# Performance work log

Measured on AMD Instinct MI355X. Metric: run time of the kernel, lower is better.

The kernel has to match this reference:

```python
import jax, jax.numpy as jnp
import numpy as np

L, D, H, F = 6, 1024, 8, 2048
B, S, IN = 4, 2048, 128
DK = D // H
EPS = 1e-6


def layer_norm(x, s, b):
    mu = jnp.mean(x, -1, keepdims=True)
    var = jnp.mean((x - mu) ** 2, -1, keepdims=True)
    return (x - mu) * jax.lax.rsqrt(var + EPS) * s + b


def rotate_every_two(x):
    x1 = x[..., ::2]
    x2 = x[..., 1::2]
    return jnp.stack([-x2, x1], axis=-1).reshape(x.shape)


def rotary_tables():
    # torchscale RetNet xpos-style angles: each freq repeated twice (interleaved)
    angle = 1.0 / (10000.0 ** jnp.linspace(0.0, 1.0, DK // 2))
    angle = jnp.repeat(angle, 2)                      # [DK]
    idx = jnp.arange(S, dtype=jnp.float32)[:, None]   # [S,1]
    return jnp.sin(idx * angle), jnp.cos(idx * angle)  # [S,DK] each


def decay_mask():
    # gamma_h = 1 - 2^(-5-h); D[h,n,m] = gamma_h^(n-m) for n>=m else 0,
    # row-normalized by sqrt(row sum) as in torchscale.
    gamma = 1.0 - 2.0 ** (-5.0 - jnp.arange(H, dtype=jnp.float32))  # [H]
    n = jnp.arange(S)
    diff = jnp.clip(n[:, None] - n[None, :], 0)                      # [S,S]
    tril = n[:, None] >= n[None, :]
    m = jnp.where(tril[None], gamma[:, None, None] ** diff[None].astype(jnp.float32), 0.0)
    return m / jnp.sqrt(jnp.sum(m, -1, keepdims=True))               # [H,S,S]


def setup_inputs() -> dict:
    key = jax.random.key(0)
    ks = iter(jax.random.split(key, 24))
    p = lambda shape: jax.random.normal(next(ks), shape, jnp.float32) * 0.02
    return {
        "x": jax.random.normal(next(ks), (B, S, IN), jnp.float32),
        "W_in": p((IN, D)), "b_in": jnp.zeros((D,), jnp.float32),
        "Wq": p((L, D, D)), "Wk": p((L, D, D)), "Wv": p((L, D, D)),
        "Wg": p((L, D, D)), "Wo": p((L, D, D)),
        "gn_g": jnp.ones((L, D), jnp.float32),
        "ln1_s": jnp.ones((L, D), jnp.float32), "ln1_b": jnp.zeros((L, D), jnp.float32),
        "ffn_W1": p((L, D, F)), "ffn_b1": jnp.zeros((L, F), jnp.float32),
        "ffn_W2": p((L, F, D)), "ffn_b2": jnp.zeros((L, D), jnp.float32),
        "ln2_s": jnp.ones((L, D), jnp.float32), "ln2_b": jnp.zeros((L, D), jnp.float32),
        "lnf_s": jnp.ones((D,), jnp.float32), "lnf_b": jnp.zeros((D,), jnp.float32),
        "W_reg": p((D, 1)), "b_reg": jnp.zeros((1,), jnp.float32),
    }


def reference(x, W_in, b_in, Wq, Wk, Wv, Wg, Wo, gn_g, ln1_s, ln1_b,
              ffn_W1, ffn_b1, ffn_W2, ffn_b2, ln2_s, ln2_b, lnf_s, lnf_b,
              W_reg, b_reg):
    sin, cos = rotary_tables()
    dmask = decay_mask()  # [H,S,S]
    h = x @ W_in + b_in   # input_embed
    for l in range(L):
        # --- multi-scale retention (pre-norm) ---
        y = layer_norm(h, ln1_s[l], ln1_b[l])
        q = (y @ Wq[l]).reshape(B, S, H, DK).transpose(0, 2, 1, 3)
        k = (y @ Wk[l]).reshape(B, S, H, DK).transpose(0, 2, 1, 3) * (DK ** -0.5)
        v = (y @ Wv[l]).reshape(B, S, H, DK).transpose(0, 2, 1, 3)
        q = q * cos + rotate_every_two(q) * sin
        k = k * cos + rotate_every_two(k) * sin
        scores = jnp.einsum('bhnd,bhmd->bhnm', q, k)
        ret = scores * dmask[None]
        ret = ret / jnp.clip(jnp.abs(ret).sum(-1, keepdims=True), 1.0, None)
        o = jnp.einsum('bhnm,bhmd->bhnd', ret, v)
        # per-head group (RMS) norm
        o = o * jax.lax.rsqrt(jnp.mean(o * o, -1, keepdims=True) + EPS)
        o = o.transpose(0, 2, 1, 3).reshape(B, S, D) * gn_g[l]
        g = y @ Wg[l]
        h = h + (jax.nn.silu(g) * o) @ Wo[l]
        # --- FFN (pre-norm) ---
        y = layer_norm(h, ln2_s[l], ln2_b[l])
        h = h + jax.nn.gelu(y @ ffn_W1[l] + ffn_b1[l]) @ ffn_W2[l] + ffn_b2[l]
    h = layer_norm(h, lnf_s, lnf_b)
    out = 1.1 * jax.nn.sigmoid(h @ W_reg + b_reg) - 0.05
    return out.squeeze(-1)  # [B,S]
```

## Files before the change

### kernel.cpp

```cpp
#include <hip/hip_runtime.h>

#define L_ 6
#define D_ 1024
#define H_ 8
#define F_ 2048
#define B_ 4
#define S_ 2048
#define IN_ 128
#define DK_ 128
#define BS_ (B_*S_)
#define D2_ 4096

typedef short bf16x8 __attribute__((ext_vector_type(8)));
typedef float f32x4 __attribute__((ext_vector_type(4)));

__device__ inline float b2f(unsigned short u){ union{unsigned int i; float f;} v; v.i = ((unsigned int)u)<<16; return v.f; }
__device__ inline unsigned short f2b(float f){ union{unsigned int i; float f;} v; v.f = f; unsigned int r = v.i + 0x7FFFu + ((v.i>>16)&1u); return (unsigned short)(r>>16); }
__device__ inline unsigned int cvtpk(float lo, float hi){
    unsigned int r; asm("v_cvt_pk_bf16_f32 %0, %1, %2" : "=v"(r) : "v"(lo), "v"(hi)); return r;
}

__device__ inline void gld16(const void* g, void* l) {
    __builtin_amdgcn_global_load_lds((const __attribute__((address_space(1))) unsigned int*)g,
                                     (__attribute__((address_space(3))) unsigned int*)l, 16, 0, 0);
}

#define GBAR() do{ asm volatile("" ::: "memory"); __builtin_amdgcn_s_barrier(); asm volatile("" ::: "memory"); }while(0)

__global__ void f32_to_bf16_k(const float* __restrict__ in, unsigned short* __restrict__ out, int n)
{
    int i = blockIdx.x*256 + threadIdx.x;
    if (i < n) out[i] = f2b(in[i]);
}

__global__ void transpose_w_k(const float* __restrict__ in, unsigned short* __restrict__ out, int R, int C, size_t ostride)
{
    __shared__ float tile[32][33];
    int z = blockIdx.z;
    const float* pi = in + (size_t)z*R*C;
    unsigned short* po = out + (size_t)z*ostride;
    int c0 = blockIdx.x*32, r0 = blockIdx.y*32;
    int tx = threadIdx.x, ty = threadIdx.y;
    #pragma unroll
    for (int i=0;i<4;i++) tile[ty+i*8][tx] = pi[(size_t)(r0+ty+i*8)*C + c0+tx];
    __syncthreads();
    #pragma unroll
    for (int i=0;i<4;i++) po[(size_t)(c0+ty+i*8)*R + r0+tx] = f2b(tile[tx][ty+i*8]);
}

__global__ void transpose_v_k(const unsigned short* __restrict__ vb, unsigned short* __restrict__ vT)
{
    __shared__ unsigned short tile[32][33];
    int z = blockIdx.z;
    int b = z >> 3, hh = z & 7;
    int s0 = blockIdx.x*32, d0 = blockIdx.y*32;
    int tx = threadIdx.x, ty = threadIdx.y;
    #pragma unroll
    for (int i=0;i<4;i++) tile[ty+i*8][tx] = vb[(size_t)(b*S_ + s0+ty+i*8)*D2_ + hh*DK_ + d0+tx];
    __syncthreads();
    #pragma unroll
    for (int i=0;i<4;i++) vT[((size_t)z*DK_ + d0+ty+i*8)*S_ + s0+tx] = tile[tx][ty+i*8];
}

__global__ void build_sincos_k(float* __restrict__ cost, float* __restrict__ sint)
{
    int id = blockIdx.x*256 + threadIdx.x;
    int s = id >> 6, i = id & 63;
    float ang = powf(10000.f, -(float)i/63.f);
    float a = (float)s * ang;
    float sv = sinf(a), cv = cosf(a);
    sint[s*DK_ + 2*i] = sv; sint[s*DK_ + 2*i+1] = sv;
    cost[s*DK_ + 2*i] = cv; cost[s*DK_ + 2*i+1] = cv;
}

__global__ void build_dnorm_k(float* __restrict__ dnorm)
{
    int id = blockIdx.x*256 + threadIdx.x;
    int h = id >> 11, n = id & (S_-1);
    double g = 1.0 - exp2((double)(-5 - h));
    double sum = (1.0 - exp(((double)(n+1))*log(g))) / (1.0 - g);
    dnorm[id] = (float)(1.0/sqrt(sum));
}

__device__ inline float bsum(float v, float* red, int t)
{
    #pragma unroll
    for (int m=32; m; m>>=1) v += __shfl_xor(v, m);
    __syncthreads();
    if ((t & 63) == 0) red[t>>6] = v;
    __syncthreads();
    return red[0]+red[1]+red[2]+red[3];
}

__global__ __launch_bounds__(256) void ln_to_bf16_k(const float* __restrict__ x, const float* __restrict__ s,
                                                    const float* __restrict__ b, unsigned short* __restrict__ y)
{
    __shared__ float red[4];
    int row = blockIdx.x, t = threadIdx.x;
    const float* xr = x + (size_t)row * D_;
    float4 v = ((const float4*)xr)[t];
    float mu = bsum(v.x+v.y+v.z+v.w, red, t) * (1.f/D_);
    float d0=v.x-mu, d1=v.y-mu, d2=v.z-mu, d3=v.w-mu;
    float var = bsum(d0*d0+d1*d1+d2*d2+d3*d3, red, t) * (1.f/D_);
    float inv = rsqrtf(var + 1e-6f);
    int c = t*4;
    float o0 = d0*inv*s[c+0] + b[c+0];
    float o1 = d1*inv*s[c+1] + b[c+1];
    float o2 = d2*inv*s[c+2] + b[c+2];
    float o3 = d3*inv*s[c+3] + b[c+3];
    unsigned long long pk = (unsigned long long)f2b(o0) | ((unsigned long long)f2b(o1)<<16)
                          | ((unsigned long long)f2b(o2)<<32) | ((unsigned long long)f2b(o3)<<48);
    *(unsigned long long*)(y + (size_t)row*D_ + c) = pk;
}

template<int MODE, int BN>
__global__ __launch_bounds__(512, 2)
void gemm6(const unsigned short* __restrict__ A,
           const unsigned short* __restrict__ Bt,
           const float* __restrict__ bias,
           void* __restrict__ Cv,
           int M, int N, int K)
{
    constexpr int BM   = 256;
    constexpr int IR   = 8;
    constexpr int JR   = BN/64;
    constexpr int ASUB = BM*64;
    constexpr int BSUB = BN*64;
    constexpr int BUFSZ= 2*ASUB + 2*BSUB;
    constexpr int AP   = 2;
    constexpr int BP   = BN/128;
    __shared__ unsigned char lds[2*BUFSZ];

    const int tid = threadIdx.x, lane = tid & 63, w = tid >> 6;
    const int r16 = lane & 15, quad = (lane >> 4) & 3;
    const int wm = w >> 2, wn = w & 3;

    const int nwg = (int)(gridDim.x * gridDim.y);
    int bid = (int)(blockIdx.y * gridDim.x + blockIdx.x);
    if ((nwg & 7) == 0) bid = (bid & 7) * (nwg >> 3) + (bid >> 3);
    const int m0 = (bid / (int)gridDim.x) * BM;
    const int n0 = (bid % (int)gridDim.x) * BN;

    const int srow = tid >> 2;
    const int schk = (tid & 3) ^ ((tid >> 3) & 3);
    const unsigned short* gA = A  + (size_t)(m0 + srow) * K + schk*8;
    const unsigned short* gB = Bt + (size_t)(n0 + srow) * K + schk*8;

    const int rchk = (quad ^ ((r16 >> 1) & 3)) * 16;
    const int aoff = (wm*128 + r16)*64 + rchk;
    const int boff = (wn*(BN/4) + r16)*64 + rchk;

    f32x4 acc[IR][JR];
    #pragma unroll
    for (int i=0;i<IR;i++)
      #pragma unroll
      for (int j=0;j<JR;j++) acc[i][j] = (f32x4){0.f,0.f,0.f,0.f};

    const int NT = K >> 6;

    auto stageA = [&](int t, int kk){
        unsigned char* dst = lds + (t&1)*BUFSZ + kk*ASUB;
        const unsigned short* src = gA + (size_t)t*64 + kk*32;
        #pragma unroll
        for (int p=0;p<AP;p++)
            gld16(src + (size_t)(p*128)*K, dst + p*8192 + tid*16);
    };
    auto stageB = [&](int t, int kk){
        unsigned char* dst = lds + (t&1)*BUFSZ + 2*ASUB + kk*BSUB;
        const unsigned short* src = gB + (size_t)t*64 + kk*32;
        #pragma unroll
        for (int p=0;p<BP;p++)
            gld16(src + (size_t)(p*128)*K, dst + p*8192 + tid*16);
    };

    stageA(0,0); stageB(0,0); stageA(0,1); stageB(0,1);
    if constexpr (BN==256) asm volatile("s_waitcnt vmcnt(4)" ::: "memory");
    else                   asm volatile("s_waitcnt vmcnt(3)" ::: "memory");
    GBAR();

    for (int t = 0; t < NT; ++t) {
        const unsigned char* cb = lds + (t&1)*BUFSZ;
        const bool pre = (t+1 < NT);
        #pragma unroll
        for (int kk = 0; kk < 2; ++kk) {
            const unsigned char* ak = cb + kk*ASUB;
            const unsigned char* bk = cb + 2*ASUB + kk*BSUB;
            if constexpr (BN == 256) {
                bf16x8 af[4], bg[JR];
                #pragma unroll
                for (int i=0;i<4;i++) af[i] = *(const bf16x8*)(ak + aoff + i*1024);
                #pragma unroll
                for (int j=0;j<JR;j++) bg[j] = *(const bf16x8*)(bk + boff + j*1024);
                if (pre) stageA(t+1, kk);
                GBAR();
                asm volatile("s_waitcnt lgkmcnt(0)" ::: "memory");
                __builtin_amdgcn_s_setprio(1);
                #pragma unroll
                for (int i=0;i<4;i++)
                  #pragma unroll
                  for (int j=0;j<JR;j++)
                    acc[i][j] = __builtin_amdgcn_mfma_f32_16x16x32_bf16(af[i], bg[j], acc[i][j], 0,0,0);
                __builtin_amdgcn_s_setprio(0);
                GBAR();
                #pragma unroll
                for (int i=0;i<4;i++) af[i] = *(const bf16x8*)(ak + aoff + (4+i)*1024);
                if (pre) stageB(t+1, kk);
                GBAR();
                asm volatile("s_waitcnt lgkmcnt(0)" ::: "memory");
                __builtin_amdgcn_s_setprio(1);
                #pragma unroll
                for (int i=0;i<4;i++)
                  #pragma unroll
                  for (int j=0;j<JR;j++)
                    acc[4+i][j] = __builtin_amdgcn_mfma_f32_16x16x32_bf16(af[i], bg[j], acc[4+i][j], 0,0,0);
                __builtin_amdgcn_s_setprio(0);
                if (pre) asm volatile("s_waitcnt vmcnt(4)" ::: "memory");
                else     asm volatile("s_waitcnt vmcnt(0)" ::: "memory");
                GBAR();
            } else {
                bf16x8 af[8], bg[JR];
                #pragma unroll
                for (int i=0;i<8;i++) af[i] = *(const bf16x8*)(ak + aoff + i*1024);
                #pragma unroll
                for (int j=0;j<JR;j++) bg[j] = *(const bf16x8*)(bk + boff + j*1024);
                if (pre) { stageA(t+1, kk); stageB(t+1, kk); }
                GBAR();
                asm volatile("s_waitcnt lgkmcnt(0)" ::: "memory");
                __builtin_amdgcn_s_setprio(1);
                #pragma unroll
                for (int i=0;i<8;i++)
                  #pragma unroll
                  for (int j=0;j<JR;j++)
                    acc[i][j] = __builtin_amdgcn_mfma_f32_16x16x32_bf16(af[i], bg[j], acc[i][j], 0,0,0);
                __builtin_amdgcn_s_setprio(0);
                if (pre) asm volatile("s_waitcnt vmcnt(3)" ::: "memory");
                else     asm volatile("s_waitcnt vmcnt(0)" ::: "memory");
                GBAR();
            }
        }
    }

    float* Cf = (float*)Cv;
    unsigned short* Cb = (unsigned short*)Cv;
    float bvs[JR];
    #pragma unroll
    for (int j=0;j<JR;j++) bvs[j] = bias ? bias[n0 + wn*(BN/4) + j*16 + r16] : 0.f;
    #pragma unroll
    for (int i=0;i<IR;i++) {
      #pragma unroll
      for (int r=0;r<4;r++) {
        const size_t crow = (size_t)(m0 + wm*128 + i*16 + quad*4 + r);
        #pragma unroll
        for (int j=0;j<JR;j++) {
          const int ccol = n0 + wn*(BN/4) + j*16 + r16;
          float v = acc[i][j][r];
          if (MODE == 0) { Cf[crow*N + ccol] = v + bvs[j]; }
          else if (MODE == 1) { Cf[crow*N + ccol] += v + bvs[j]; }
          else if (MODE == 2) { Cb[crow*N + ccol] = f2b(v); }
          else {
            v += bvs[j];
            float t3 = tanhf(0.7978845608028654f*(v + 0.044715f*v*v*v));
            Cb[crow*N + ccol] = f2b(0.5f*v*(1.f + t3));
          }
        }
      }
    }
}

__global__ __launch_bounds__(256) void rope_qk_k(unsigned short* __restrict__ qkvg,
                                                 const float* __restrict__ cost, const float* __restrict__ sint)
{
    int id = blockIdx.x*256 + threadIdx.x;
    int row = id >> 9;
    int d = (id & 511) * 2;
    int s = row & (S_-1);
    int dk = d & (DK_-1);
    float c0 = cost[s*DK_ + dk],   s0 = sint[s*DK_ + dk];
    float c1 = cost[s*DK_ + dk+1], s1 = sint[s*DK_ + dk+1];
    size_t off = (size_t)row*D2_ + d;
    unsigned int qu = *(unsigned int*)(qkvg + off);
    float q0 = b2f((unsigned short)(qu & 0xffffu)), q1 = b2f((unsigned short)(qu >> 16));
    float r0 = q0*c0 - q1*s0;
    float r1 = q1*c1 + q0*s1;
    *(unsigned int*)(qkvg + off) = (unsigned int)f2b(r0) | ((unsigned int)f2b(r1) << 16);
    const float sc = 0.08838834764831845f;
    unsigned int ku = *(unsigned int*)(qkvg + off + 1024);
    float k0 = b2f((unsigned short)(ku & 0xffffu))*sc, k1 = b2f((unsigned short)(ku >> 16))*sc;
    float t0 = k0*c0 - k1*s0;
    float t1 = k1*c1 + k0*s1;
    *(unsigned int*)(qkvg + off + 1024) = (unsigned int)f2b(t0) | ((unsigned int)f2b(t1) << 16);
}

__global__ __launch_bounds__(256, 2) void retention_k(const unsigned short* __restrict__ qk_base,
    const unsigned short* __restrict__ vT, const float* __restrict__ dnorm,
    const float* __restrict__ gng, unsigned short* __restrict__ attnin)
{
    __shared__ __align__(16) unsigned char lds[75776];
    const int Lf = (int)(blockIdx.y * gridDim.x + blockIdx.x);
    const int kx = Lf & 7, mm = Lf >> 3;
    const int bh = 4*kx + (mm >> 4);
    const int pr = mm & 15;
    const int b = bh >> 3, hh = bh & 7;
    const int tid = threadIdx.x, lane = tid & 63, w = tid >> 6;
    const int r16 = lane & 15, quad = lane >> 4;

    const float l2g = log2f(1.f - exp2f(-5.f - (float)hh));
    const int ithr = (int)(45.f / (-l2g));
    const unsigned int mkr = (r16 & 7) << 4;

    const int mk2  = ((tid >> 4) & 7) << 4;
    const int mkv2 = ((tid >> 3) & 7) << 4;
    const unsigned short* ksrc = qk_base + 1024 + ((size_t)(b*S_) + (tid>>4))*D2_ + hh*DK_
                                + ((((tid&15)*16) ^ mk2) >> 1);
    const unsigned short* vsrc = vT + ((size_t)bh*DK_ + (tid>>3))*S_ + ((((tid&7)*16) ^ mkv2) >> 1);

    float Aarr[4];
    #pragma unroll
    for (int r=0;r<4;r++) Aarr[r] = exp2f(l2g * (float)(63 - (w*16 + quad*4 + r)));

    float* dsums = (float*)(lds + 73728);
    float* ssums = (float*)(lds + 74752);

    auto stage = [&](int c2, int kt2){
        const unsigned short* s0 = ksrc + (size_t)kt2*64*D2_;
        #pragma unroll
        for (int i=0;i<4;i++)
            gld16(s0 + (size_t)i*16*D2_, lds + c2*16384 + i*4096 + w*1024);
        const unsigned short* s1 = vsrc + kt2*64;
        #pragma unroll
        for (int j=0;j<4;j++)
            gld16(s1 + (size_t)j*32*S_, lds + 32768 + c2*16384 + j*4096 + w*1024);
    };

    int cur = 0;

    #pragma unroll 1
    for (int seg = 0; seg < 2; ++seg) {
        const int qt = seg ? pr : (31 - pr);
        const int n0 = qt * 64;
        const int kt_start = max(0, (n0 - ithr) >> 6);

        bf16x8 qf[4][4];
        const unsigned short* qptr = qk_base + ((size_t)(b*S_ + n0 + r16))*D2_ + hh*DK_;
        #pragma unroll
        for (int qtl=0;qtl<4;qtl++)
          #pragma unroll
          for (int c=0;c<4;c++) qf[qtl][c] = *(const bf16x8*)(qptr + qtl*16*D2_ + c*32 + quad*8);

        f32x4 oacc[4][2];
        #pragma unroll
        for (int qtl=0;qtl<4;qtl++)
          #pragma unroll
          for (int dt=0;dt<2;dt++) oacc[qtl][dt] = (f32x4){0.f,0.f,0.f,0.f};
        float dsum[4] = {0.f,0.f,0.f,0.f};

        stage(cur, kt_start);

        #pragma unroll 1
        for (int kt = kt_start; kt <= qt; ++kt) {
            if (kt < qt) { stage(cur^1, kt+1); asm volatile("s_waitcnt vmcnt(8)" ::: "memory"); }
            else         { asm volatile("s_waitcnt vmcnt(0)" ::: "memory"); }
            GBAR();

            const unsigned char* kb = lds + cur*16384;
            bf16x8 kf[4];
            #pragma unroll
            for (int c=0;c<4;c++)
                kf[c] = *(const bf16x8*)(kb + (w*16 + r16)*256 + ((c*64 + quad*16) ^ mkr));
            f32x4 sf[4];
            #pragma unroll
            for (int qtl=0;qtl<4;qtl++) sf[qtl] = (f32x4){0.f,0.f,0.f,0.f};
            __builtin_amdgcn_s_setprio(1);
            #pragma unroll
            for (int c=0;c<4;c++)
              #pragma unroll
              for (int qtl=0;qtl<4;qtl++)
                sf[qtl] = __builtin_amdgcn_mfma_f32_16x16x32_bf16(kf[c], qf[qtl][c], sf[qtl], 0,0,0);
            __builtin_amdgcn_s_setprio(0);

            const bool diag = (kt == qt);
            #pragma unroll
            for (int qtl=0;qtl<4;qtl++) {
                float Bq = exp2f(l2g * (float)(n0 + qtl*16 + r16 - kt*64 - 63));
                float pv[4];
                #pragma unroll
                for (int r=0;r<4;r++) {
                    float p = sf[qtl][r] * Aarr[r] * Bq;
                    if (diag && (w*16 + quad*4 + r > qtl*16 + r16)) p = 0.f;
                    dsum[qtl] += fabsf(p);
                    pv[r] = p;
                }
                unsigned long long pk = (unsigned long long)cvtpk(pv[0], pv[1])
                                      | ((unsigned long long)cvtpk(pv[2], pv[3]) << 32);
                *(unsigned long long*)(lds + 65536 + (qtl*16 + r16)*128 + ((w*32 + quad*8) ^ mkr)) = pk;
            }
            asm volatile("s_waitcnt lgkmcnt(0)" ::: "memory");
            GBAR();

            const unsigned char* vb = lds + 32768 + cur*16384;
            bf16x8 pa[4][2], vf[2][2];
            #pragma unroll
            for (int qtl=0;qtl<4;qtl++)
              #pragma unroll
              for (int ks=0;ks<2;ks++)
                pa[qtl][ks] = *(const bf16x8*)(lds + 65536 + (qtl*16 + r16)*128 + ((ks*64 + quad*16) ^ mkr));
            #pragma unroll
            for (int dt=0;dt<2;dt++)
              #pragma unroll
              for (int ks=0;ks<2;ks++)
                vf[dt][ks] = *(const bf16x8*)(vb + (w*32 + dt*16 + r16)*128 + ((ks*64 + quad*16) ^ mkr));
            __builtin_amdgcn_s_setprio(1);
            #pragma unroll
            for (int qtl=0;qtl<4;qtl++)
              #pragma unroll
              for (int dt=0;dt<2;dt++)
                #pragma unroll
                for (int ks=0;ks<2;ks++)
                  oacc[qtl][dt] = __builtin_amdgcn_mfma_f32_16x16x32_bf16(pa[qtl][ks], vf[dt][ks], oacc[qtl][dt], 0,0,0);
            __builtin_amdgcn_s_setprio(0);
            GBAR();
            cur ^= 1;
        }

        #pragma unroll
        for (int qtl=0;qtl<4;qtl++) {
            float dv = dsum[qtl];
            dv += __shfl_xor(dv, 16); dv += __shfl_xor(dv, 32);
            if (lane < 16) dsums[w*64 + qtl*16 + r16] = dv;
        }
        __syncthreads();
        float scl[4][4], pss[4][4];
        #pragma unroll
        for (int qtl=0;qtl<4;qtl++) {
            #pragma unroll
            for (int r=0;r<4;r++) {
                int nl = qtl*16 + quad*4 + r;
                float dv = dsums[nl] + dsums[64+nl] + dsums[128+nl] + dsums[192+nl];
                float nr = dnorm[hh*S_ + n0 + nl];
                float sc = nr / fmaxf(1.f, dv * nr);
                scl[qtl][r] = sc;
                float s2 = 0.f;
                #pragma unroll
                for (int dt=0;dt<2;dt++) { float t = oacc[qtl][dt][r]*sc; s2 += t*t; }
                s2 += __shfl_xor(s2,1); s2 += __shfl_xor(s2,2);
                s2 += __shfl_xor(s2,4); s2 += __shfl_xor(s2,8);
                pss[qtl][r] = s2;
            }
        }
        if (r16 == 0) {
            #pragma unroll
            for (int qtl=0;qtl<4;qtl++)
              #pragma unroll
              for (int r=0;r<4;r++)
                ssums[w*64 + qtl*16 + quad*4 + r] = pss[qtl][r];
        }
        __syncthreads();
        #pragma unroll
        for (int qtl=0;qtl<4;qtl++) {
            float rms[4];
            #pragma unroll
            for (int r=0;r<4;r++) {
                int nl = qtl*16 + quad*4 + r;
                float s2 = ssums[nl] + ssums[64+nl] + ssums[128+nl] + ssums[192+nl];
                rms[r] = rsqrtf(s2*(1.f/DK_) + 1e-6f);
            }
            #pragma unroll
            for (int dt=0;dt<2;dt++) {
                int d = w*32 + dt*16 + r16;
                float gg = gng[hh*DK_ + d];
                #pragma unroll
                for (int r=0;r<4;r++) {
                    int n = n0 + qtl*16 + quad*4 + r;
                    float gv = b2f(qk_base[(size_t)(b*S_ + n)*D2_ + 3072 + hh*DK_ + d]);
                    float sg = gv / (1.f + expf(-gv));
                    float ov = oacc[qtl][dt][r]*scl[qtl][r]*rms[r]*gg;
                    attnin[(size_t)(b*S_ + n)*D_ + hh*DK_ + d] = f2b(ov*sg);
                }
            }
        }
        __syncthreads();
    }
}

__global__ __launch_bounds__(256) void head_out_k(const float* __restrict__ h, const float* __restrict__ s,
    const float* __restrict__ b, const float* __restrict__ wreg, const float* __restrict__ breg,
    float* __restrict__ out)
{
    __shared__ float red[4];
    int row = blockIdx.x, t = threadIdx.x;
    const float* xr = h + (size_t)row*D_;
    float4 v = ((const float4*)xr)[t];
    float mu = bsum(v.x+v.y+v.z+v.w, red, t) * (1.f/D_);
    float d0=v.x-mu, d1=v.y-mu, d2=v.z-mu, d3=v.w-mu;
    float var = bsum(d0*d0+d1*d1+d2*d2+d3*d3, red, t) * (1.f/D_);
    float inv = rsqrtf(var + 1e-6f);
    int c = t*4;
    float dot = (d0*inv*s[c+0]+b[c+0])*wreg[c+0] + (d1*inv*s[c+1]+b[c+1])*wreg[c+1]
              + (d2*inv*s[c+2]+b[c+2])*wreg[c+2] + (d3*inv*s[c+3]+b[c+3])*wreg[c+3];
    dot = bsum(dot, red, t);
    if (t == 0) out[row] = 1.1f / (1.f + expf(-(dot + breg[0]))) - 0.05f;
}

extern "C" void kernel_launch(void* const* d_in, const int* in_sizes, int n_in,
                              void* d_out, int out_size, void* d_ws, size_t ws_size,
                              hipStream_t stream)
{
    (void)in_sizes; (void)n_in; (void)out_size; (void)ws_size;
    const float* x    = (const float*)d_in[0];
    const float* W_in = (const float*)d_in[1];
    const float* b_in = (const float*)d_in[2];
    const float* Wq   = (const float*)d_in[3];
    const float* Wk   = (const float*)d_in[4];
    const float* Wv   = (const float*)d_in[5];
    const float* Wg   = (const float*)d_in[6];
    const float* Wo   = (const float*)d_in[7];
    const float* gn_g = (const float*)d_in[8];
    const float* ln1s = (const float*)d_in[9];
    const float* ln1b = (const float*)d_in[10];
    const float* W1   = (const float*)d_in[11];
    const float* b1   = (const float*)d_in[12];
    const float* W2   = (const float*)d_in[13];
    const float* b2   = (const float*)d_in[14];
    const float* ln2s = (const float*)d_in[15];
    const float* ln2b = (const float*)d_in[16];
    const float* lnfs = (const float*)d_in[17];
    const float* lnfb = (const float*)d_in[18];
    const float* Wreg = (const float*)d_in[19];
    const float* breg = (const float*)d_in[20];

    char* ws = (char*)d_ws;
    size_t off = 0;
    auto alloc = [&](size_t bytes) { char* p = ws + off; off += (bytes + 255) & ~(size_t)255; return p; };

    const size_t DD = (size_t)D_*D_;
    unsigned short* wqkvgT = (unsigned short*)alloc((size_t)L_*4*DD*2);
    unsigned short* woT  = (unsigned short*)alloc((size_t)L_*DD*2);
    unsigned short* w1T  = (unsigned short*)alloc((size_t)L_*D_*F_*2);
    unsigned short* w2T  = (unsigned short*)alloc((size_t)L_*D_*F_*2);
    unsigned short* winT = (unsigned short*)alloc((size_t)D_*IN_*2);
    unsigned short* x_bf = (unsigned short*)alloc((size_t)BS_*IN_*2);
    float*          hbuf = (float*)alloc((size_t)BS_*D_*4);
    unsigned short* y_bf = (unsigned short*)alloc((size_t)BS_*D_*2);
    unsigned short* qkvg = (unsigned short*)alloc((size_t)BS_*D2_*2);
    unsigned short* vTb  = (unsigned short*)alloc((size_t)BS_*D_*2);
    float*          cost = (float*)alloc((size_t)S_*DK_*4);
    float*          sint = (float*)alloc((size_t)S_*DK_*4);
    float*          dnrm = (float*)alloc((size_t)H_*S_*4);
    unsigned short* attn = y_bf;
    unsigned short* midb = qkvg;

    dim3 tb(32, 8);

    f32_to_bf16_k<<<(BS_*IN_)/256, 256, 0, stream>>>(x, x_bf, BS_*IN_);
    transpose_w_k<<<dim3(32,32,L_), tb, 0, stream>>>(Wq, wqkvgT + 0*DD, D_, D_, 4*DD);
    transpose_w_k<<<dim3(32,32,L_), tb, 0, stream>>>(Wk, wqkvgT + 1*DD, D_, D_, 4*DD);
    transpose_w_k<<<dim3(32,32,L_), tb, 0, stream>>>(Wv, wqkvgT + 2*DD, D_, D_, 4*DD);
    transpose_w_k<<<dim3(32,32,L_), tb, 0, stream>>>(Wg, wqkvgT + 3*DD, D_, D_, 4*DD);
    transpose_w_k<<<dim3(32,32,L_), tb, 0, stream>>>(Wo, woT, D_, D_, DD);
    transpose_w_k<<<dim3(64,32,L_), tb, 0, stream>>>(W1, w1T, D_, F_, (size_t)D_*F_);
    transpose_w_k<<<dim3(32,64,L_), tb, 0, stream>>>(W2, w2T, F_, D_, (size_t)D_*F_);
    transpose_w_k<<<dim3(32, 4, 1), tb, 0, stream>>>(W_in, winT, IN_, D_, (size_t)D_*IN_);
    build_sincos_k<<<(S_*64)/256, 256, 0, stream>>>(cost, sint);
    build_dnorm_k<<<(H_*S_)/256, 256, 0, stream>>>(dnrm);

    gemm6<0,128><<<dim3(D_/128, BS_/256), 512, 0, stream>>>(x_bf, winT, b_in, hbuf, BS_, D_, IN_);

    for (int l = 0; l < L_; ++l) {
        ln_to_bf16_k<<<BS_, 256, 0, stream>>>(hbuf, ln1s + l*D_, ln1b + l*D_, y_bf);
        gemm6<2,256><<<dim3(D2_/256, BS_/256), 512, 0, stream>>>(y_bf, wqkvgT + (size_t)l*4*DD, nullptr, qkvg, BS_, D2_, D_);
        rope_qk_k<<<(BS_*D_/2)/256, 256, 0, stream>>>(qkvg, cost, sint);
        transpose_v_k<<<dim3(S_/32, DK_/32, B_*H_), tb, 0, stream>>>(qkvg + 2048, vTb);
        retention_k<<<dim3(16, B_*H_), 256, 0, stream>>>(qkvg, vTb, dnrm, gn_g + l*D_, attn);
        gemm6<1,128><<<dim3(D_/128, BS_/256), 512, 0, stream>>>(attn, woT + (size_t)l*DD, nullptr, hbuf, BS_, D_, D_);
        ln_to_bf16_k<<<BS_, 256, 0, stream>>>(hbuf, ln2s + l*D_, ln2b + l*D_, y_bf);
        gemm6<3,256><<<dim3(F_/256, BS_/256), 512, 0, stream>>>(y_bf, w1T + (size_t)l*D_*F_, b1 + l*F_, midb, BS_, F_, D_);
        gemm6<1,128><<<dim3(D_/128, BS_/256), 512, 0, stream>>>(midb, w2T + (size_t)l*D_*F_, b2 + l*D_, hbuf, BS_, D_, F_);
    }

    head_out_k<<<BS_, 256, 0, stream>>>(hbuf, lnfs, lnfb, Wreg, breg, (float*)d_out);
}
```

Baseline: 1.983 ms.

## Fuse RoPE into V transpose and templatize GEMM tile height

Removes the standalone RoPE kernel and applies rotary embedding to Q and K inside the V-transpose kernel, so one launch and one extra pass over the QKVG buffer go away. The GEMM kernel now takes the M tile size as a template parameter. The Wo, FFN1 and FFN2 GEMMs switch to 128x128 tiles, giving more workgroups on the device at the cost of less data reuse per tile. The BN=256 path also issues its B prefetch together with the A prefetch instead of later in the step. The vmcnt wait counts are generalized to match the new number of loads per stage.

```diff
diff --git a/kernel.cpp b/kernel.cpp
--- a/kernel.cpp
+++ b/kernel.cpp
@@ -48,15 +48,42 @@
     for (int i=0;i<4;i++) po[(size_t)(c0+ty+i*8)*R + r0+tx] = f2b(tile[tx][ty+i*8]);
 }
 
-__global__ void transpose_v_k(const unsigned short* __restrict__ vb, unsigned short* __restrict__ vT)
+__global__ void rope_vt_k(unsigned short* __restrict__ qkvg, unsigned short* __restrict__ vT,
+                          const float* __restrict__ cost, const float* __restrict__ sint)
 {
     __shared__ unsigned short tile[32][33];
     int z = blockIdx.z;
     int b = z >> 3, hh = z & 7;
     int s0 = blockIdx.x*32, d0 = blockIdx.y*32;
     int tx = threadIdx.x, ty = threadIdx.y;
+    const unsigned short* vb = qkvg + 2048;
     #pragma unroll
     for (int i=0;i<4;i++) tile[ty+i*8][tx] = vb[(size_t)(b*S_ + s0+ty+i*8)*D2_ + hh*DK_ + d0+tx];
+
+    int t = ty*32 + tx;
+    #pragma unroll
+    for (int it=0; it<2; ++it) {
+        int idx = it*256 + t;
+        int row = idx >> 4;
+        int pr  = idx & 15;
+        int s  = s0 + row;
+        int dk = d0 + pr*2;
+        float c0 = cost[s*DK_ + dk],   sn0 = sint[s*DK_ + dk];
+        float c1 = cost[s*DK_ + dk+1], sn1 = sint[s*DK_ + dk+1];
+        size_t off = (size_t)(b*S_ + s)*D2_ + hh*DK_ + dk;
+        unsigned int qu = *(unsigned int*)(qkvg + off);
+        float q0 = b2f((unsigned short)(qu & 0xffffu)), q1 = b2f((unsigned short)(qu >> 16));
+        float r0 = q0*c0 - q1*sn0;
+        float r1 = q1*c1 + q0*sn1;
+        *(unsigned int*)(qkvg + off) = (unsigned int)f2b(r0) | ((unsigned int)f2b(r1) << 16);
+        const float sc = 0.08838834764831845f;
+        unsigned int ku = *(unsigned int*)(qkvg + off + 1024);
+        float k0 = b2f((unsigned short)(ku & 0xffffu))*sc, k1 = b2f((unsigned short)(ku >> 16))*sc;
+        float t0 = k0*c0 - k1*sn0;
+        float t1 = k1*c1 + k0*sn1;
+        *(unsigned int*)(qkvg + off + 1024) = (unsigned int)f2b(t0) | ((unsigned int)f2b(t1) << 16);
+    }
+
     __syncthreads();
     #pragma unroll
     for (int i=0;i<4;i++) vT[((size_t)z*DK_ + d0+ty+i*8)*S_ + s0+tx] = tile[tx][ty+i*8];
@@ -113,7 +140,7 @@
     *(unsigned long long*)(y + (size_t)row*D_ + c) = pk;
 }
 
-template<int MODE, int BN>
+template<int MODE, int BM, int BN>
 __global__ __launch_bounds__(512, 2)
 void gemm6(const unsigned short* __restrict__ A,
            const unsigned short* __restrict__ Bt,
@@ -121,14 +148,14 @@
            void* __restrict__ Cv,
            int M, int N, int K)
 {
-    constexpr int BM   = 256;
-    constexpr int IR   = 8;
+    constexpr int IR   = BM/2/16;
     constexpr int JR   = BN/64;
     constexpr int ASUB = BM*64;
     constexpr int BSUB = BN*64;
     constexpr int BUFSZ= 2*ASUB + 2*BSUB;
-    constexpr int AP   = 2;
+    constexpr int AP   = BM/128;
     constexpr int BP   = BN/128;
+    constexpr int Sa   = AP + BP;
     __shared__ unsigned char lds[2*BUFSZ];
 
     const int tid = threadIdx.x, lane = tid & 63, w = tid >> 6;
@@ -147,7 +174,7 @@
     const unsigned short* gB = Bt + (size_t)(n0 + srow) * K + schk*8;
 
     const int rchk = (quad ^ ((r16 >> 1) & 3)) * 16;
-    const int aoff = (wm*128 + r16)*64 + rchk;
+    const int aoff = (wm*(BM/2) + r16)*64 + rchk;
     const int boff = (wn*(BN/4) + r16)*64 + rchk;
 
     f32x4 acc[IR][JR];
@@ -173,9 +200,12 @@
             gld16(src + (size_t)(p*128)*K, dst + p*8192 + tid*16);
     };
 
+    #define WAIT_SA() do{ if constexpr (Sa==4) asm volatile("s_waitcnt vmcnt(4)" ::: "memory"); \
+                          else if constexpr (Sa==3) asm volatile("s_waitcnt vmcnt(3)" ::: "memory"); \
+                          else asm volatile("s_waitcnt vmcnt(2)" ::: "memory"); }while(0)
+
     stageA(0,0); stageB(0,0); stageA(0,1); stageB(0,1);
-    if constexpr (BN==256) asm volatile("s_waitcnt vmcnt(4)" ::: "memory");
-    else                   asm volatile("s_waitcnt vmcnt(3)" ::: "memory");
+    WAIT_SA();
     GBAR();
 
     for (int t = 0; t < NT; ++t) {
@@ -191,7 +221,7 @@
                 for (int i=0;i<4;i++) af[i] = *(const bf16x8*)(ak + aoff + i*1024);
                 #pragma unroll
                 for (int j=0;j<JR;j++) bg[j] = *(const bf16x8*)(bk + boff + j*1024);
-                if (pre) stageA(t+1, kk);
+                if (pre) { stageA(t+1, kk); stageB(t+1, kk); }
                 GBAR();
                 asm volatile("s_waitcnt lgkmcnt(0)" ::: "memory");
                 __builtin_amdgcn_s_setprio(1);
@@ -204,7 +234,6 @@
                 GBAR();
                 #pragma unroll
                 for (int i=0;i<4;i++) af[i] = *(const bf16x8*)(ak + aoff + (4+i)*1024);
-                if (pre) stageB(t+1, kk);
                 GBAR();
                 asm volatile("s_waitcnt lgkmcnt(0)" ::: "memory");
                 __builtin_amdgcn_s_setprio(1);
@@ -214,13 +243,13 @@
                   for (int j=0;j<JR;j++)
                     acc[4+i][j] = __builtin_amdgcn_mfma_f32_16x16x32_bf16(af[i], bg[j], acc[4+i][j], 0,0,0);
                 __builtin_amdgcn_s_setprio(0);
-                if (pre) asm volatile("s_waitcnt vmcnt(4)" ::: "memory");
+                if (pre) { WAIT_SA(); }
                 else     asm volatile("s_waitcnt vmcnt(0)" ::: "memory");
                 GBAR();
             } else {
-                bf16x8 af[8], bg[JR];
-                #pragma unroll
-                for (int i=0;i<8;i++) af[i] = *(const bf16x8*)(ak + aoff + i*1024);
+                bf16x8 af[IR], bg[JR];
+                #pragma unroll
+                for (int i=0;i<IR;i++) af[i] = *(const bf16x8*)(ak + aoff + i*1024);
                 #pragma unroll
                 for (int j=0;j<JR;j++) bg[j] = *(const bf16x8*)(bk + boff + j*1024);
                 if (pre) { stageA(t+1, kk); stageB(t+1, kk); }
@@ -228,17 +257,18 @@
                 asm volatile("s_waitcnt lgkmcnt(0)" ::: "memory");
                 __builtin_amdgcn_s_setprio(1);
                 #pragma unroll
-                for (int i=0;i<8;i++)
+                for (int i=0;i<IR;i++)
                   #pragma unroll
                   for (int j=0;j<JR;j++)
                     acc[i][j] = __builtin_amdgcn_mfma_f32_16x16x32_bf16(af[i], bg[j], acc[i][j], 0,0,0);
                 __builtin_amdgcn_s_setprio(0);
-                if (pre) asm volatile("s_waitcnt vmcnt(3)" ::: "memory");
+                if (pre) { WAIT_SA(); }
                 else     asm volatile("s_waitcnt vmcnt(0)" ::: "memory");
                 GBAR();
             }
         }
     }
+    #undef WAIT_SA
 
     float* Cf = (float*)Cv;
     unsigned short* Cb = (unsigned short*)Cv;
@@ -249,7 +279,7 @@
     for (int i=0;i<IR;i++) {
       #pragma unroll
       for (int r=0;r<4;r++) {
-        const size_t crow = (size_t)(m0 + wm*128 + i*16 + quad*4 + r);
+        const size_t crow = (size_t)(m0 + wm*(BM/2) + i*16 + quad*4 + r);
         #pragma unroll
         for (int j=0;j<JR;j++) {
           const int ccol = n0 + wn*(BN/4) + j*16 + r16;
@@ -265,30 +295,6 @@
         }
       }
     }
-}
-
-__global__ __launch_bounds__(256) void rope_qk_k(unsigned short* __restrict__ qkvg,
-                                                 const float* __restrict__ cost, const float* __restrict__ sint)
-{
-    int id = blockIdx.x*256 + threadIdx.x;
-    int row = id >> 9;
-    int d = (id & 511) * 2;
-    int s = row & (S_-1);
-    int dk = d & (DK_-1);
-    float c0 = cost[s*DK_ + dk],   s0 = sint[s*DK_ + dk];
-    float c1 = cost[s*DK_ + dk+1], s1 = sint[s*DK_ + dk+1];
-    size_t off = (size_t)row*D2_ + d;
-    unsigned int qu = *(unsigned int*)(qkvg + off);
-    float q0 = b2f((unsigned short)(qu & 0xffffu)), q1 = b2f((unsigned short)(qu >> 16));
-    float r0 = q0*c0 - q1*s0;
-    float r1 = q1*c1 + q0*s1;
-    *(unsigned int*)(qkvg + off) = (unsigned int)f2b(r0) | ((unsigned int)f2b(r1) << 16);
-    const float sc = 0.08838834764831845f;
-    unsigned int ku = *(unsigned int*)(qkvg + off + 1024);
-    float k0 = b2f((unsigned short)(ku & 0xffffu))*sc, k1 = b2f((unsigned short)(ku >> 16))*sc;
-    float t0 = k0*c0 - k1*s0;
-    float t1 = k1*c1 + k0*s1;
-    *(unsigned int*)(qkvg + off + 1024) = (unsigned int)f2b(t0) | ((unsigned int)f2b(t1) << 16);
 }
 
 __global__ __launch_bounds__(256, 2) void retention_k(const unsigned short* __restrict__ qk_base,
@@ -563,18 +569,17 @@
     build_sincos_k<<<(S_*64)/256, 256, 0, stream>>>(cost, sint);
     build_dnorm_k<<<(H_*S_)/256, 256, 0, stream>>>(dnrm);
 
-    gemm6<0,128><<<dim3(D_/128, BS_/256), 512, 0, stream>>>(x_bf, winT, b_in, hbuf, BS_, D_, IN_);
+    gemm6<0,128,128><<<dim3(D_/128, BS_/128), 512, 0, stream>>>(x_bf, winT, b_in, hbuf, BS_, D_, IN_);
 
     for (int l = 0; l < L_; ++l) {
         ln_to_bf16_k<<<BS_, 256, 0, stream>>>(hbuf, ln1s + l*D_, ln1b + l*D_, y_bf);
-        gemm6<2,256><<<dim3(D2_/256, BS_/256), 512, 0, stream>>>(y_bf, wqkvgT + (size_t)l*4*DD, nullptr, qkvg, BS_, D2_, D_);
-        rope_qk_k<<<(BS_*D_/2)/256, 256, 0, stream>>>(qkvg, cost, sint);
-        transpose_v_k<<<dim3(S_/32, DK_/32, B_*H_), tb, 0, stream>>>(qkvg + 2048, vTb);
+        gemm6<2,256,256><<<dim3(D2_/256, BS_/256), 512, 0, stream>>>(y_bf, wqkvgT + (size_t)l*4*DD, nullptr, qkvg, BS_, D2_, D_);
+        rope_vt_k<<<dim3(S_/32, DK_/32, B_*H_), tb, 0, stream>>>(qkvg, vTb, cost, sint);
         retention_k<<<dim3(16, B_*H_), 256, 0, stream>>>(qkvg, vTb, dnrm, gn_g + l*D_, attn);
-        gemm6<1,128><<<dim3(D_/128, BS_/256), 512, 0, stream>>>(attn, woT + (size_t)l*DD, nullptr, hbuf, BS_, D_, D_);
+        gemm6<1,128,128><<<dim3(D_/128, BS_/128), 512, 0, stream>>>(attn, woT + (size_t)l*DD, nullptr, hbuf, BS_, D_, D_);
         ln_to_bf16_k<<<BS_, 256, 0, stream>>>(hbuf, ln2s + l*D_, ln2b + l*D_, y_bf);
-        gemm6<3,256><<<dim3(F_/256, BS_/256), 512, 0, stream>>>(y_bf, w1T + (size_t)l*D_*F_, b1 + l*F_, midb, BS_, F_, D_);
-        gemm6<1,128><<<dim3(D_/128, BS_/256), 512, 0, stream>>>(midb, w2T + (size_t)l*D_*F_, b2 + l*D_, hbuf, BS_, D_, F_);
+        gemm6<3,128,128><<<dim3(F_/128, BS_/128), 512, 0, stream>>>(y_bf, w1T + (size_t)l*D_*F_, b1 + l*F_, midb, BS_, F_, D_);
+        gemm6<1,128,128><<<dim3(D_/128, BS_/128), 512, 0, stream>>>(midb, w2T + (size_t)l*D_*F_, b2 + l*D_, hbuf, BS_, D_, F_);
     }
 
     head_out_k<<<BS_, 256, 0, stream>>>(hbuf, lnfs, lnfb, Wreg, breg, (float*)d_out);
```

New measurement: 1.916 ms. 1.04x faster.
